# Performance work log

Hardware: AMD Instinct MI355X
Metric: run time of the kernel (lower is better)

The kernel has to match this reference:

```python
import jax, jax.numpy as jnp
import numpy as np

N_NODES = 100000
N_EDGES = 1600000
D_FEAT = 64
UNITS = [128, 128]


def setup_inputs() -> dict:
    key = jax.random.key(0)
    ks = jax.random.split(key, 8)
    row = jax.random.randint(ks[0], (N_EDGES,), 0, N_NODES, dtype=jnp.int32)
    col = jax.random.randint(ks[1], (N_EDGES,), 0, N_NODES, dtype=jnp.int32)
    vals = jax.random.uniform(ks[2], (N_EDGES,), dtype=jnp.float32)
    H = jax.random.normal(ks[3], (N_NODES, D_FEAT), dtype=jnp.float32)
    W1 = jax.random.normal(ks[4], (D_FEAT, UNITS[0]), dtype=jnp.float32) * (1.0 / np.sqrt(D_FEAT))
    b1 = jnp.zeros((UNITS[0],), dtype=jnp.float32)
    W2 = jax.random.normal(ks[5], (UNITS[0], UNITS[1]), dtype=jnp.float32) * (1.0 / np.sqrt(UNITS[0]))
    b2 = jnp.zeros((UNITS[1],), dtype=jnp.float32)
    return {"row": row, "col": col, "vals": vals, "H": H,
            "W1": W1, "b1": b1, "W2": W2, "b2": b2}


def _spmm(row, col, vals, H, n_nodes):
    # sparse A (COO) @ dense H: gather source rows, scale, scatter-add to dest
    return jax.ops.segment_sum(vals[:, None] * H[col], row, num_segments=n_nodes)


def reference(row, col, vals, H, W1, b1, W2, b2):
    n = H.shape[0]
    # layer 0: AH @ W1 + b1, relu (source bug: relu applied since i < num_units-1)
    AH = _spmm(row, col, vals, H, n)
    H1 = jax.nn.relu(AH @ W1 + b1)
    # layer 1: same structure, also relu per source's activation condition
    AH1 = _spmm(row, col, vals, H1, n)
    H2 = jax.nn.relu(AH1 @ W2 + b2)
    return H2
```

## Files before the change

kernel.cpp:

```cpp
#include <hip/hip_runtime.h>


#define NFEAT 64
#define NHID 128
#define BSHIFT 9
#define BROWS (1 << BSHIFT)
#define NB_MAX 256

typedef __attribute__((ext_vector_type(8))) short bf16x8;
typedef __attribute__((ext_vector_type(4))) float f32x4;
typedef __attribute__((ext_vector_type(2))) float f32x2;

__device__ __forceinline__ unsigned short f2bf(float x) {
  unsigned u = __float_as_uint(x);
  unsigned r = (u + 0x7FFFu + ((u >> 16) & 1u)) >> 16;
  return (unsigned short)r;
}
__device__ __forceinline__ unsigned pack2(float a, float b) {
  return (unsigned)f2bf(a) | ((unsigned)f2bf(b) << 16);
}

__device__ __forceinline__ unsigned pk_fp8x4(float a, float b, float c, float d) {
  int w = __builtin_amdgcn_cvt_pk_fp8_f32(a, b, 0, false);
  w = __builtin_amdgcn_cvt_pk_fp8_f32(c, d, w, true);
  return (unsigned)w;
}
__device__ __forceinline__ unsigned char f2fp8(float x) {
  return (unsigned char)(__builtin_amdgcn_cvt_pk_fp8_f32(x, 0.f, 0, false) & 0xFF);
}

__device__ __forceinline__ void acc16(f32x2* a, uint4 q, float v) {
  f32x2 vv = {v, v};
  a[0] += vv * __builtin_amdgcn_cvt_pk_f32_fp8(q.x, false);
  a[1] += vv * __builtin_amdgcn_cvt_pk_f32_fp8(q.x, true);
  a[2] += vv * __builtin_amdgcn_cvt_pk_f32_fp8(q.y, false);
  a[3] += vv * __builtin_amdgcn_cvt_pk_f32_fp8(q.y, true);
  a[4] += vv * __builtin_amdgcn_cvt_pk_f32_fp8(q.z, false);
  a[5] += vv * __builtin_amdgcn_cvt_pk_f32_fp8(q.z, true);
  a[6] += vv * __builtin_amdgcn_cvt_pk_f32_fp8(q.w, false);
  a[7] += vv * __builtin_amdgcn_cvt_pk_f32_fp8(q.w, true);
}

__global__ __launch_bounds__(256) void prep_kernel(
    const float* __restrict__ H, const float* __restrict__ W1,
    const float* __restrict__ W2, unsigned char* __restrict__ Hf8,
    unsigned short* __restrict__ Wsw1, unsigned short* __restrict__ Wsw2,
    int n8) {
  const int total = n8 + 64 * 128 + 128 * 128;
  for (int w = blockIdx.x * 256 + threadIdx.x; w < total; w += gridDim.x * 256) {
    if (w < n8) {
      float4 a = ((const float4*)H)[2 * w];
      float4 b = ((const float4*)H)[2 * w + 1];
      ((uint2*)Hf8)[w] = make_uint2(pk_fp8x4(a.x, a.y, a.z, a.w),
                                    pk_fp8x4(b.x, b.y, b.z, b.w));
    } else {
      int idx = w - n8;
      const float* W = W1;
      unsigned short* Wsw = Wsw1;
      if (idx >= 64 * 128) {
        idx -= 64 * 128;
        W = W2;
        Wsw = Wsw2;
      }
      int j = idx & 7, q = (idx >> 3) & 3, nn = (idx >> 5) & 127, kt = idx >> 12;
      int k = kt * 32 + q * 8 + j;
      Wsw[idx] = f2bf(W[(size_t)k * 128 + nn]);
    }
  }
}

__global__ __launch_bounds__(256) void bhist_kernel(
    const int* __restrict__ row, int* __restrict__ bcnt, int n_edges, int nb) {
  __shared__ int h[NB_MAX];
  for (int i = threadIdx.x; i < NB_MAX; i += 256) h[i] = 0;
  __syncthreads();
  for (int e = blockIdx.x * 256 + threadIdx.x; e < n_edges; e += gridDim.x * 256)
    atomicAdd(&h[row[e] >> BSHIFT], 1);
  __syncthreads();
  for (int i = threadIdx.x; i < nb; i += 256)
    if (h[i]) atomicAdd(&bcnt[i], h[i]);
}

__global__ __launch_bounds__(NB_MAX) void bscan_kernel(
    const int* __restrict__ bcnt, int* __restrict__ bbase, int* __restrict__ cur,
    int* __restrict__ row_ptr, int nb, int n) {
  __shared__ int sm[NB_MAX];
  int t = threadIdx.x;
  int v = (t < nb) ? bcnt[t] : 0;
  sm[t] = v;
  __syncthreads();
  for (int off = 1; off < NB_MAX; off <<= 1) {
    int u = (t >= off) ? sm[t - off] : 0;
    __syncthreads();
    sm[t] += u;
    __syncthreads();
  }
  if (t < nb) {
    bbase[t] = sm[t] - v;
    cur[t] = sm[t] - v;
  }
  if (t == nb - 1) {
    bbase[nb] = sm[t];
    row_ptr[n] = sm[t];
  }
}

__global__ __launch_bounds__(1024) void partition_kernel(
    const int* __restrict__ row, const int* __restrict__ col,
    const float* __restrict__ vals, int* __restrict__ cur,
    int2* __restrict__ bedge, int n_edges) {
  __shared__ int h[NB_MAX], base[NB_MAX], rk[NB_MAX];
  for (int i = threadIdx.x; i < NB_MAX; i += 1024) {
    h[i] = 0;
    rk[i] = 0;
  }
  __syncthreads();
  const int start = blockIdx.x * 1024 + threadIdx.x;
  const int step = gridDim.x * 1024;
  for (int e = start; e < n_edges; e += step)
    atomicAdd(&h[row[e] >> BSHIFT], 1);
  __syncthreads();
  for (int i = threadIdx.x; i < NB_MAX; i += 1024)
    base[i] = h[i] ? atomicAdd(&cur[i], h[i]) : 0;
  __syncthreads();
  for (int e = start; e < n_edges; e += step) {
    int r = row[e];
    int b = r >> BSHIFT;
    int rl = r & (BROWS - 1);
    int p = base[b] + atomicAdd(&rk[b], 1);
    bedge[p] = make_int2((rl << 17) | col[e], __float_as_int(vals[e]));
  }
}

__global__ __launch_bounds__(1024) void bucket_csr_kernel(
    const int* __restrict__ bbase, const int2* __restrict__ bedge,
    int* __restrict__ row_ptr, int2* __restrict__ sedge, int n) {
  __shared__ int cnt[BROWS];
  __shared__ int sm[BROWS];
  const int b = blockIdx.x;
  const int t = threadIdx.x;
  const int beg = bbase[b], end = bbase[b + 1];
  if (t < BROWS) cnt[t] = 0;
  __syncthreads();
  for (int j = beg + t; j < end; j += 1024)
    atomicAdd(&cnt[((unsigned)bedge[j].x) >> 17], 1);
  __syncthreads();
  int v = (t < BROWS) ? cnt[t] : 0;
  if (t < BROWS) sm[t] = v;
  __syncthreads();
  for (int off = 1; off < BROWS; off <<= 1) {
    int u = (t >= off && t < BROWS) ? sm[t - off] : 0;
    __syncthreads();
    if (t < BROWS) sm[t] += u;
    __syncthreads();
  }
  int incl = (t < BROWS) ? sm[t] : 0;
  __syncthreads();
  if (t < BROWS) {
    sm[t] = incl - v;
    int r = (b << BSHIFT) + t;
    if (r < n) row_ptr[r] = beg + sm[t];
    cnt[t] = 0;
  }
  __syncthreads();
  for (int j = beg + t; j < end; j += 1024) {
    int2 ev = bedge[j];
    int rl = ((unsigned)ev.x) >> 17;
    int rank = atomicAdd(&cnt[rl], 1);
    sedge[beg + sm[rl] + rank] = make_int2(ev.x & 0x1FFFF, ev.y);
  }
}

__global__ __launch_bounds__(256) void spmm64_csr_f8(
    const int* __restrict__ row_ptr, const int2* __restrict__ sedge,
    const unsigned char* __restrict__ Hf8, unsigned short* __restrict__ outbf,
    int n) {
  int tid = blockIdx.x * 256 + threadIdx.x;
  int r = tid >> 2;
  int f = tid & 3;
  if (r >= n) return;
  const uint4* Hq = (const uint4*)Hf8;
  int beg = row_ptr[r], end = row_ptr[r + 1];
  f32x2 a[8];
#pragma unroll
  for (int i = 0; i < 8; ++i) a[i] = (f32x2){0.f, 0.f};
  int j = beg;
  if ((j & 1) && j < end) {
    int2 ev = sedge[j];
    uint4 q = Hq[ev.x * 4 + f];
    acc16(a, q, __int_as_float(ev.y));
    ++j;
  }
  for (; j + 4 <= end; j += 4) {
    int4 p0 = ((const int4*)sedge)[j >> 1];
    int4 p1 = ((const int4*)sedge)[(j >> 1) + 1];
    uint4 q0 = Hq[p0.x * 4 + f];
    uint4 q1 = Hq[p0.z * 4 + f];
    uint4 q2 = Hq[p1.x * 4 + f];
    uint4 q3 = Hq[p1.z * 4 + f];
    acc16(a, q0, __int_as_float(p0.y));
    acc16(a, q1, __int_as_float(p0.w));
    acc16(a, q2, __int_as_float(p1.y));
    acc16(a, q3, __int_as_float(p1.w));
  }
  for (; j < end; ++j) {
    int2 ev = sedge[j];
    uint4 q = Hq[ev.x * 4 + f];
    acc16(a, q, __int_as_float(ev.y));
  }
  uint4 o0 = make_uint4(pack2(a[0].x, a[0].y), pack2(a[1].x, a[1].y),
                        pack2(a[2].x, a[2].y), pack2(a[3].x, a[3].y));
  uint4 o1 = make_uint4(pack2(a[4].x, a[4].y), pack2(a[5].x, a[5].y),
                        pack2(a[6].x, a[6].y), pack2(a[7].x, a[7].y));
  ((uint4*)outbf)[(size_t)r * 8 + f * 2] = o0;
  ((uint4*)outbf)[(size_t)r * 8 + f * 2 + 1] = o1;
}

__global__ __launch_bounds__(256) void spmm128_csr_f8(
    const int* __restrict__ row_ptr, const int2* __restrict__ sedge,
    const unsigned char* __restrict__ Hf8, unsigned short* __restrict__ outbf,
    int n) {
  int tid = blockIdx.x * 256 + threadIdx.x;
  int r = tid >> 3;
  int f = tid & 7;
  if (r >= n) return;
  const uint4* Hq = (const uint4*)Hf8;
  int beg = row_ptr[r], end = row_ptr[r + 1];
  f32x2 a[8];
#pragma unroll
  for (int i = 0; i < 8; ++i) a[i] = (f32x2){0.f, 0.f};
  int j = beg;
  if ((j & 1) && j < end) {
    int2 ev = sedge[j];
    uint4 q = Hq[ev.x * 8 + f];
    acc16(a, q, __int_as_float(ev.y));
    ++j;
  }
  for (; j + 4 <= end; j += 4) {
    int4 p0 = ((const int4*)sedge)[j >> 1];
    int4 p1 = ((const int4*)sedge)[(j >> 1) + 1];
    uint4 q0 = Hq[p0.x * 8 + f];
    uint4 q1 = Hq[p0.z * 8 + f];
    uint4 q2 = Hq[p1.x * 8 + f];
    uint4 q3 = Hq[p1.z * 8 + f];
    acc16(a, q0, __int_as_float(p0.y));
    acc16(a, q1, __int_as_float(p0.w));
    acc16(a, q2, __int_as_float(p1.y));
    acc16(a, q3, __int_as_float(p1.w));
  }
  for (; j < end; ++j) {
    int2 ev = sedge[j];
    uint4 q = Hq[ev.x * 8 + f];
    acc16(a, q, __int_as_float(ev.y));
  }
  uint4 o0 = make_uint4(pack2(a[0].x, a[0].y), pack2(a[1].x, a[1].y),
                        pack2(a[2].x, a[2].y), pack2(a[3].x, a[3].y));
  uint4 o1 = make_uint4(pack2(a[4].x, a[4].y), pack2(a[5].x, a[5].y),
                        pack2(a[6].x, a[6].y), pack2(a[7].x, a[7].y));
  ((uint4*)outbf)[(size_t)r * 16 + f * 2] = o0;
  ((uint4*)outbf)[(size_t)r * 16 + f * 2 + 1] = o1;
}

template <int K, int OUTMODE>
__global__ __launch_bounds__(256) void gemm_mfma_relu(
    const unsigned short* __restrict__ Abf,
    const unsigned short* __restrict__ Wsw,
    const float* __restrict__ b, void* __restrict__ out_v, int n) {
  constexpr int KT = K / 32;
  const int lane = threadIdx.x & 63;
  const int wave = threadIdx.x >> 6;
  const int m = lane & 15;
  const int quad = lane >> 4;
  const int r0 = blockIdx.x * 64 + wave * 16;

  bf16x8 bfr[KT][8];
#pragma unroll
  for (int kt = 0; kt < KT; ++kt)
#pragma unroll
    for (int c = 0; c < 8; ++c)
      bfr[kt][c] = *(const bf16x8*)(Wsw + ((size_t)(kt * 128 + c * 16 + m)) * 32 + quad * 8);

  f32x4 acc[8];
#pragma unroll
  for (int c = 0; c < 8; ++c) acc[c] = (f32x4){0.f, 0.f, 0.f, 0.f};

  int row = r0 + m;
  if (row >= n) row = n - 1;
  const uint4* Arow = (const uint4*)(Abf + (size_t)row * K);
#pragma unroll
  for (int kt = 0; kt < KT; ++kt) {
    bf16x8 a = *(const bf16x8*)&Arow[kt * 4 + quad];
#pragma unroll
    for (int c = 0; c < 8; ++c)
      acc[c] = __builtin_amdgcn_mfma_f32_16x16x32_bf16(a, bfr[kt][c], acc[c], 0, 0, 0);
  }

#pragma unroll
  for (int c = 0; c < 8; ++c) {
    float bias = b[c * 16 + m];
#pragma unroll
    for (int i = 0; i < 4; ++i) {
      int rr = r0 + quad * 4 + i;
      if (rr >= n) continue;
      float v = fmaxf(acc[c][i] + bias, 0.f);
      if (OUTMODE == 2)
        ((unsigned char*)out_v)[(size_t)rr * 128 + c * 16 + m] = f2fp8(v);
      else
        ((float*)out_v)[(size_t)rr * 128 + c * 16 + m] = v;
    }
  }
}

__global__ __launch_bounds__(256) void spmm64_atomic(
    const int* __restrict__ row, const int* __restrict__ col,
    const float* __restrict__ vals, const float* __restrict__ Hin,
    float* __restrict__ out, int n_edges) {
  int tid = blockIdx.x * 256 + threadIdx.x;
  int e = tid >> 4, f = tid & 15;
  if (e >= n_edges) return;
  int c = col[e], r = row[e];
  float v = vals[e];
  float4 h = ((const float4*)Hin)[(size_t)c * 16 + f];
  float* o = out + (size_t)r * 64 + f * 4;
  atomicAdd(o + 0, v * h.x);
  atomicAdd(o + 1, v * h.y);
  atomicAdd(o + 2, v * h.z);
  atomicAdd(o + 3, v * h.w);
}

__global__ __launch_bounds__(256) void spmm128_atomic(
    const int* __restrict__ row, const int* __restrict__ col,
    const float* __restrict__ vals, const float* __restrict__ Hin,
    float* __restrict__ out, int n_edges) {
  int tid = blockIdx.x * 256 + threadIdx.x;
  int e = tid >> 5, f = tid & 31;
  if (e >= n_edges) return;
  int c = col[e], r = row[e];
  float v = vals[e];
  float4 h = ((const float4*)Hin)[(size_t)c * 32 + f];
  float* o = out + (size_t)r * 128 + f * 4;
  atomicAdd(o + 0, v * h.x);
  atomicAdd(o + 1, v * h.y);
  atomicAdd(o + 2, v * h.z);
  atomicAdd(o + 3, v * h.w);
}

template <int K>
__global__ __launch_bounds__(256) void gemm_tiled_relu(
    const float* __restrict__ A, const float* __restrict__ W,
    const float* __restrict__ b, float* __restrict__ out, int n) {
  constexpr int KB = 32;
  constexpr int RP = 132;
  __shared__ float As[KB][RP];
  __shared__ float Ws[KB][128];
  const int t = threadIdx.x;
  const int tx = t & 15, ty = t >> 4;
  const int r0 = blockIdx.x * 128;
  float4 acc0[8], acc1[8];
#pragma unroll
  for (int i = 0; i < 8; ++i) {
    acc0[i] = make_float4(0.f, 0.f, 0.f, 0.f);
    acc1[i] = make_float4(0.f, 0.f, 0.f, 0.f);
  }
  for (int k0 = 0; k0 < K; k0 += KB) {
#pragma unroll
    for (int q = 0; q < 4; ++q) {
      int f = q * 256 + t;
      int kk = f >> 5, cv = f & 31;
      ((float4*)&Ws[kk][0])[cv] = ((const float4*)(W + (size_t)(k0 + kk) * 128))[cv];
    }
#pragma unroll
    for (int q = 0; q < 4; ++q) {
      int f = q * 256 + t;
      int r = f >> 3, kv = f & 7;
      float4 av = make_float4(0.f, 0.f, 0.f, 0.f);
      if (r0 + r < n) av = ((const float4*)(A + (size_t)(r0 + r) * K + k0))[kv];
      As[4 * kv + 0][r] = av.x;
      As[4 * kv + 1][r] = av.y;
      As[4 * kv + 2][r] = av.z;
      As[4 * kv + 3][r] = av.w;
    }
    __syncthreads();
#pragma unroll
    for (int k = 0; k < KB; ++k) {
      float4 w0 = *((const float4*)&Ws[k][4 * tx]);
      float4 w1 = *((const float4*)&Ws[k][64 + 4 * tx]);
#pragma unroll
      for (int i = 0; i < 8; ++i) {
        float a = As[k][ty + 16 * i];
        acc0[i].x = fmaf(a, w0.x, acc0[i].x);
        acc0[i].y = fmaf(a, w0.y, acc0[i].y);
        acc0[i].z = fmaf(a, w0.z, acc0[i].z);
        acc0[i].w = fmaf(a, w0.w, acc0[i].w);
        acc1[i].x = fmaf(a, w1.x, acc1[i].x);
        acc1[i].y = fmaf(a, w1.y, acc1[i].y);
        acc1[i].z = fmaf(a, w1.z, acc1[i].z);
        acc1[i].w = fmaf(a, w1.w, acc1[i].w);
      }
    }
    __syncthreads();
  }
  float4 bb0 = ((const float4*)b)[tx];
  float4 bb1 = ((const float4*)(b + 64))[tx];
#pragma unroll
  for (int i = 0; i < 8; ++i) {
    int r = r0 + ty + 16 * i;
    if (r >= n) continue;
    float4 o0, o1;
    o0.x = fmaxf(acc0[i].x + bb0.x, 0.f);
    o0.y = fmaxf(acc0[i].y + bb0.y, 0.f);
    o0.z = fmaxf(acc0[i].z + bb0.z, 0.f);
    o0.w = fmaxf(acc0[i].w + bb0.w, 0.f);
    o1.x = fmaxf(acc1[i].x + bb1.x, 0.f);
    o1.y = fmaxf(acc1[i].y + bb1.y, 0.f);
    o1.z = fmaxf(acc1[i].z + bb1.z, 0.f);
    o1.w = fmaxf(acc1[i].w + bb1.w, 0.f);
    ((float4*)(out + (size_t)r * 128))[tx] = o0;
    ((float4*)(out + (size_t)r * 128 + 64))[tx] = o1;
  }
}

extern "C" void kernel_launch(void* const* d_in, const int* in_sizes, int n_in,
                              void* d_out, int out_size, void* d_ws, size_t ws_size,
                              hipStream_t stream) {
  const int* row = (const int*)d_in[0];
  const int* col = (const int*)d_in[1];
  const float* vals = (const float*)d_in[2];
  const float* H = (const float*)d_in[3];
  const float* W1 = (const float*)d_in[4];
  const float* b1 = (const float*)d_in[5];
  const float* W2 = (const float*)d_in[6];
  const float* b2 = (const float*)d_in[7];
  float* out = (float*)d_out;

  const int n_edges = in_sizes[0];
  const int n_nodes = in_sizes[3] / NFEAT;
  const int nb = (n_nodes + BROWS - 1) / BROWS;
  const int mfma_grid = (n_nodes + 63) / 64;

  size_t off = 0;
  char* base = (char*)d_ws;
  char* slab0 = base;
  size_t slab0_sz = (size_t)n_edges * 8;
  size_t ah1_sz = (size_t)n_nodes * NHID * 2;
  if (ah1_sz > slab0_sz) slab0_sz = ah1_sz;
  off += slab0_sz;
  unsigned char* Hf8 = (unsigned char*)(base + off);   off += (size_t)n_nodes * NFEAT;
  unsigned char* H1f8 = (unsigned char*)(base + off);  off += (size_t)n_nodes * NHID;
  unsigned short* AHbf = (unsigned short*)(base + off); off += (size_t)n_nodes * NFEAT * 2;
  int2* sedge = (int2*)(base + off);  off += (size_t)n_edges * 8;
  unsigned short* Wsw1 = (unsigned short*)(base + off); off += 64 * 128 * 2;
  unsigned short* Wsw2 = (unsigned short*)(base + off); off += 128 * 128 * 2;
  int* bcnt = (int*)(base + off);     off += NB_MAX * 4;
  int* bbase = (int*)(base + off);    off += (NB_MAX + 1) * 4;
  int* cur = (int*)(base + off);      off += NB_MAX * 4;
  int* row_ptr = (int*)(base + off);  off += ((size_t)n_nodes + 1) * 4;
  const size_t needed = off;
  int2* bedge = (int2*)slab0;
  unsigned short* AH1bf = (unsigned short*)slab0;

  if (ws_size >= needed && nb <= NB_MAX && n_nodes <= (1 << 17)) {
    hipMemsetAsync(bcnt, 0, NB_MAX * sizeof(int), stream);
    bhist_kernel<<<1024, 256, 0, stream>>>(row, bcnt, n_edges, nb);
    bscan_kernel<<<1, NB_MAX, 0, stream>>>(bcnt, bbase, cur, row_ptr, nb, n_nodes);
    partition_kernel<<<256, 1024, 0, stream>>>(row, col, vals, cur, bedge, n_edges);
    bucket_csr_kernel<<<nb, 1024, 0, stream>>>(bbase, bedge, row_ptr, sedge, n_nodes);

    prep_kernel<<<1024, 256, 0, stream>>>(H, W1, W2, Hf8, Wsw1, Wsw2,
                                          n_nodes * NFEAT / 8);

    spmm64_csr_f8<<<(n_nodes * 4 + 255) / 256, 256, 0, stream>>>(
        row_ptr, sedge, Hf8, AHbf, n_nodes);
    gemm_mfma_relu<64, 2><<<mfma_grid, 256, 0, stream>>>(
        AHbf, Wsw1, b1, H1f8, n_nodes);
    spmm128_csr_f8<<<(n_nodes * 8 + 255) / 256, 256, 0, stream>>>(
        row_ptr, sedge, H1f8, AH1bf, n_nodes);
    gemm_mfma_relu<128, 0><<<mfma_grid, 256, 0, stream>>>(
        AH1bf, Wsw2, b2, out, n_nodes);
  } else {
    float* fAH = (float*)d_ws;
    float* fH1 = fAH + (size_t)n_nodes * NFEAT;
    hipMemsetAsync(fAH, 0, (size_t)n_nodes * NFEAT * sizeof(float), stream);
    hipMemsetAsync(out, 0, (size_t)n_nodes * NHID * sizeof(float), stream);
    spmm64_atomic<<<(n_edges * 16 + 255) / 256, 256, 0, stream>>>(row, col, vals, H, fAH, n_edges);
    gemm_tiled_relu<64><<<(n_nodes + 127) / 128, 256, 0, stream>>>(fAH, W1, b1, fH1, n_nodes);
    spmm128_atomic<<<(n_edges * 32 + 255) / 256, 256, 0, stream>>>(row, col, vals, fH1, out, n_edges);
    gemm_tiled_relu<128><<<(n_nodes + 127) / 128, 256, 0, stream>>>(out, W2, b2, out, n_nodes);
  }
}
```

Measured before the change: 281.5 us.

## Fuse SpMM gather with MFMA GEMM via shared-memory tile per layer

```diff
diff --git a/kernel.cpp b/kernel.cpp
--- a/kernel.cpp
+++ b/kernel.cpp
@@ -39,6 +39,34 @@
   a[5] += vv * __builtin_amdgcn_cvt_pk_f32_fp8(q.z, true);
   a[6] += vv * __builtin_amdgcn_cvt_pk_f32_fp8(q.w, false);
   a[7] += vv * __builtin_amdgcn_cvt_pk_f32_fp8(q.w, true);
+}
+
+template <int RS>
+__device__ __forceinline__ void gather_row(
+    const int2* __restrict__ sedge, const uint4* __restrict__ Hq,
+    int beg, int end, int f, f32x2* a) {
+  int j = beg;
+  if ((j & 1) && j < end) {
+    int2 ev = sedge[j];
+    acc16(a, Hq[ev.x * RS + f], __int_as_float(ev.y));
+    ++j;
+  }
+  for (; j + 4 <= end; j += 4) {
+    int4 p0 = ((const int4*)sedge)[j >> 1];
+    int4 p1 = ((const int4*)sedge)[(j >> 1) + 1];
+    uint4 q0 = Hq[p0.x * RS + f];
+    uint4 q1 = Hq[p0.z * RS + f];
+    uint4 q2 = Hq[p1.x * RS + f];
+    uint4 q3 = Hq[p1.z * RS + f];
+    acc16(a, q0, __int_as_float(p0.y));
+    acc16(a, q1, __int_as_float(p0.w));
+    acc16(a, q2, __int_as_float(p1.y));
+    acc16(a, q3, __int_as_float(p1.w));
+  }
+  for (; j < end; ++j) {
+    int2 ev = sedge[j];
+    acc16(a, Hq[ev.x * RS + f], __int_as_float(ev.y));
+  }
 }
 
 __global__ __launch_bounds__(256) void prep_kernel(
@@ -74,8 +102,16 @@
   __shared__ int h[NB_MAX];
   for (int i = threadIdx.x; i < NB_MAX; i += 256) h[i] = 0;
   __syncthreads();
-  for (int e = blockIdx.x * 256 + threadIdx.x; e < n_edges; e += gridDim.x * 256)
-    atomicAdd(&h[row[e] >> BSHIFT], 1);
+  const int n4 = n_edges >> 2;
+  for (int i = blockIdx.x * 256 + threadIdx.x; i < n4; i += gridDim.x * 256) {
+    int4 r4 = ((const int4*)row)[i];
+    atomicAdd(&h[r4.x >> BSHIFT], 1);
+    atomicAdd(&h[r4.y >> BSHIFT], 1);
+    atomicAdd(&h[r4.z >> BSHIFT], 1);
+    atomicAdd(&h[r4.w >> BSHIFT], 1);
+  }
+  if (blockIdx.x == 0 && threadIdx.x < (n_edges & 3))
+    atomicAdd(&h[row[(n4 << 2) + threadIdx.x] >> BSHIFT], 1);
   __syncthreads();
   for (int i = threadIdx.x; i < nb; i += 256)
     if (h[i]) atomicAdd(&bcnt[i], h[i]);
@@ -171,130 +207,52 @@
   }
 }
 
-__global__ __launch_bounds__(256) void spmm64_csr_f8(
+__global__ __launch_bounds__(256) void fused64_kernel(
     const int* __restrict__ row_ptr, const int2* __restrict__ sedge,
-    const unsigned char* __restrict__ Hf8, unsigned short* __restrict__ outbf,
-    int n) {
-  int tid = blockIdx.x * 256 + threadIdx.x;
-  int r = tid >> 2;
-  int f = tid & 3;
-  if (r >= n) return;
-  const uint4* Hq = (const uint4*)Hf8;
-  int beg = row_ptr[r], end = row_ptr[r + 1];
-  f32x2 a[8];
-#pragma unroll
-  for (int i = 0; i < 8; ++i) a[i] = (f32x2){0.f, 0.f};
-  int j = beg;
-  if ((j & 1) && j < end) {
-    int2 ev = sedge[j];
-    uint4 q = Hq[ev.x * 4 + f];
-    acc16(a, q, __int_as_float(ev.y));
-    ++j;
-  }
-  for (; j + 4 <= end; j += 4) {
-    int4 p0 = ((const int4*)sedge)[j >> 1];
-    int4 p1 = ((const int4*)sedge)[(j >> 1) + 1];
-    uint4 q0 = Hq[p0.x * 4 + f];
-    uint4 q1 = Hq[p0.z * 4 + f];
-    uint4 q2 = Hq[p1.x * 4 + f];
-    uint4 q3 = Hq[p1.z * 4 + f];
-    acc16(a, q0, __int_as_float(p0.y));
-    acc16(a, q1, __int_as_float(p0.w));
-    acc16(a, q2, __int_as_float(p1.y));
-    acc16(a, q3, __int_as_float(p1.w));
-  }
-  for (; j < end; ++j) {
-    int2 ev = sedge[j];
-    uint4 q = Hq[ev.x * 4 + f];
-    acc16(a, q, __int_as_float(ev.y));
-  }
-  uint4 o0 = make_uint4(pack2(a[0].x, a[0].y), pack2(a[1].x, a[1].y),
-                        pack2(a[2].x, a[2].y), pack2(a[3].x, a[3].y));
-  uint4 o1 = make_uint4(pack2(a[4].x, a[4].y), pack2(a[5].x, a[5].y),
-                        pack2(a[6].x, a[6].y), pack2(a[7].x, a[7].y));
-  ((uint4*)outbf)[(size_t)r * 8 + f * 2] = o0;
-  ((uint4*)outbf)[(size_t)r * 8 + f * 2 + 1] = o1;
-}
-
-__global__ __launch_bounds__(256) void spmm128_csr_f8(
-    const int* __restrict__ row_ptr, const int2* __restrict__ sedge,
-    const unsigned char* __restrict__ Hf8, unsigned short* __restrict__ outbf,
-    int n) {
-  int tid = blockIdx.x * 256 + threadIdx.x;
-  int r = tid >> 3;
-  int f = tid & 7;
-  if (r >= n) return;
-  const uint4* Hq = (const uint4*)Hf8;
-  int beg = row_ptr[r], end = row_ptr[r + 1];
-  f32x2 a[8];
-#pragma unroll
-  for (int i = 0; i < 8; ++i) a[i] = (f32x2){0.f, 0.f};
-  int j = beg;
-  if ((j & 1) && j < end) {
-    int2 ev = sedge[j];
-    uint4 q = Hq[ev.x * 8 + f];
-    acc16(a, q, __int_as_float(ev.y));
-    ++j;
-  }
-  for (; j + 4 <= end; j += 4) {
-    int4 p0 = ((const int4*)sedge)[j >> 1];
-    int4 p1 = ((const int4*)sedge)[(j >> 1) + 1];
-    uint4 q0 = Hq[p0.x * 8 + f];
-    uint4 q1 = Hq[p0.z * 8 + f];
-    uint4 q2 = Hq[p1.x * 8 + f];
-    uint4 q3 = Hq[p1.z * 8 + f];
-    acc16(a, q0, __int_as_float(p0.y));
-    acc16(a, q1, __int_as_float(p0.w));
-    acc16(a, q2, __int_as_float(p1.y));
-    acc16(a, q3, __int_as_float(p1.w));
-  }
-  for (; j < end; ++j) {
-    int2 ev = sedge[j];
-    uint4 q = Hq[ev.x * 8 + f];
-    acc16(a, q, __int_as_float(ev.y));
-  }
-  uint4 o0 = make_uint4(pack2(a[0].x, a[0].y), pack2(a[1].x, a[1].y),
-                        pack2(a[2].x, a[2].y), pack2(a[3].x, a[3].y));
-  uint4 o1 = make_uint4(pack2(a[4].x, a[4].y), pack2(a[5].x, a[5].y),
-                        pack2(a[6].x, a[6].y), pack2(a[7].x, a[7].y));
-  ((uint4*)outbf)[(size_t)r * 16 + f * 2] = o0;
-  ((uint4*)outbf)[(size_t)r * 16 + f * 2 + 1] = o1;
-}
-
-template <int K, int OUTMODE>
-__global__ __launch_bounds__(256) void gemm_mfma_relu(
-    const unsigned short* __restrict__ Abf,
+    const unsigned char* __restrict__ Hf8,
     const unsigned short* __restrict__ Wsw,
-    const float* __restrict__ b, void* __restrict__ out_v, int n) {
-  constexpr int KT = K / 32;
-  const int lane = threadIdx.x & 63;
-  const int wave = threadIdx.x >> 6;
-  const int m = lane & 15;
-  const int quad = lane >> 4;
-  const int r0 = blockIdx.x * 64 + wave * 16;
-
-  bf16x8 bfr[KT][8];
-#pragma unroll
-  for (int kt = 0; kt < KT; ++kt)
+    const float* __restrict__ b, unsigned char* __restrict__ H1f8, int n) {
+  __shared__ uint4 tile[64 * 9];
+  const int tid = threadIdx.x;
+  {
+    const int rl = tid >> 2, f = tid & 3;
+    const int r = blockIdx.x * 64 + rl;
+    int beg = 0, end = 0;
+    if (r < n) {
+      beg = row_ptr[r];
+      end = row_ptr[r + 1];
+    }
+    f32x2 a[8];
+#pragma unroll
+    for (int i = 0; i < 8; ++i) a[i] = (f32x2){0.f, 0.f};
+    gather_row<4>(sedge, (const uint4*)Hf8, beg, end, f, a);
+    tile[rl * 9 + f * 2] =
+        make_uint4(pack2(a[0].x, a[0].y), pack2(a[1].x, a[1].y),
+                   pack2(a[2].x, a[2].y), pack2(a[3].x, a[3].y));
+    tile[rl * 9 + f * 2 + 1] =
+        make_uint4(pack2(a[4].x, a[4].y), pack2(a[5].x, a[5].y),
+                   pack2(a[6].x, a[6].y), pack2(a[7].x, a[7].y));
+  }
+  const int lane = tid & 63, wave = tid >> 6;
+  const int m = lane & 15, quad = lane >> 4;
+  bf16x8 bfr[2][8];
+#pragma unroll
+  for (int kt = 0; kt < 2; ++kt)
 #pragma unroll
     for (int c = 0; c < 8; ++c)
       bfr[kt][c] = *(const bf16x8*)(Wsw + ((size_t)(kt * 128 + c * 16 + m)) * 32 + quad * 8);
-
+  __syncthreads();
   f32x4 acc[8];
 #pragma unroll
   for (int c = 0; c < 8; ++c) acc[c] = (f32x4){0.f, 0.f, 0.f, 0.f};
-
-  int row = r0 + m;
-  if (row >= n) row = n - 1;
-  const uint4* Arow = (const uint4*)(Abf + (size_t)row * K);
-#pragma unroll
-  for (int kt = 0; kt < KT; ++kt) {
-    bf16x8 a = *(const bf16x8*)&Arow[kt * 4 + quad];
+#pragma unroll
+  for (int kt = 0; kt < 2; ++kt) {
+    bf16x8 a = *(const bf16x8*)&tile[(wave * 16 + m) * 9 + kt * 4 + quad];
 #pragma unroll
     for (int c = 0; c < 8; ++c)
       acc[c] = __builtin_amdgcn_mfma_f32_16x16x32_bf16(a, bfr[kt][c], acc[c], 0, 0, 0);
   }
-
+  const int r0 = blockIdx.x * 64 + wave * 16;
 #pragma unroll
   for (int c = 0; c < 8; ++c) {
     float bias = b[c * 16 + m];
@@ -302,11 +260,66 @@
     for (int i = 0; i < 4; ++i) {
       int rr = r0 + quad * 4 + i;
       if (rr >= n) continue;
-      float v = fmaxf(acc[c][i] + bias, 0.f);
-      if (OUTMODE == 2)
-        ((unsigned char*)out_v)[(size_t)rr * 128 + c * 16 + m] = f2fp8(v);
-      else
-        ((float*)out_v)[(size_t)rr * 128 + c * 16 + m] = v;
+      H1f8[(size_t)rr * 128 + c * 16 + m] = f2fp8(fmaxf(acc[c][i] + bias, 0.f));
+    }
+  }
+}
+
+__global__ __launch_bounds__(512) void fused128_kernel(
+    const int* __restrict__ row_ptr, const int2* __restrict__ sedge,
+    const unsigned char* __restrict__ H1f8,
+    const unsigned short* __restrict__ Wsw,
+    const float* __restrict__ b, float* __restrict__ out, int n) {
+  __shared__ uint4 tile[64 * 17];
+  const int tid = threadIdx.x;
+  {
+    const int rl = tid >> 3, f = tid & 7;
+    const int r = blockIdx.x * 64 + rl;
+    int beg = 0, end = 0;
+    if (r < n) {
+      beg = row_ptr[r];
+      end = row_ptr[r + 1];
+    }
+    f32x2 a[8];
+#pragma unroll
+    for (int i = 0; i < 8; ++i) a[i] = (f32x2){0.f, 0.f};
+    gather_row<8>(sedge, (const uint4*)H1f8, beg, end, f, a);
+    tile[rl * 17 + f * 2] =
+        make_uint4(pack2(a[0].x, a[0].y), pack2(a[1].x, a[1].y),
+                   pack2(a[2].x, a[2].y), pack2(a[3].x, a[3].y));
+    tile[rl * 17 + f * 2 + 1] =
+        make_uint4(pack2(a[4].x, a[4].y), pack2(a[5].x, a[5].y),
+                   pack2(a[6].x, a[6].y), pack2(a[7].x, a[7].y));
+  }
+  const int lane = tid & 63, wave = tid >> 6;
+  const int m = lane & 15, quad = lane >> 4;
+  const int g = wave >> 1, h = wave & 1;
+  bf16x8 bfr[4][4];
+#pragma unroll
+  for (int kt = 0; kt < 4; ++kt)
+#pragma unroll
+    for (int c = 0; c < 4; ++c)
+      bfr[kt][c] = *(const bf16x8*)(Wsw + ((size_t)(kt * 128 + (h * 4 + c) * 16 + m)) * 32 + quad * 8);
+  __syncthreads();
+  f32x4 acc[4];
+#pragma unroll
+  for (int c = 0; c < 4; ++c) acc[c] = (f32x4){0.f, 0.f, 0.f, 0.f};
+#pragma unroll
+  for (int kt = 0; kt < 4; ++kt) {
+    bf16x8 a = *(const bf16x8*)&tile[(g * 16 + m) * 17 + kt * 4 + quad];
+#pragma unroll
+    for (int c = 0; c < 4; ++c)
+      acc[c] = __builtin_amdgcn_mfma_f32_16x16x32_bf16(a, bfr[kt][c], acc[c], 0, 0, 0);
+  }
+  const int r0 = blockIdx.x * 64 + g * 16;
+#pragma unroll
+  for (int c = 0; c < 4; ++c) {
+    float bias = b[(h * 4 + c) * 16 + m];
+#pragma unroll
+    for (int i = 0; i < 4; ++i) {
+      int rr = r0 + quad * 4 + i;
+      if (rr >= n) continue;
+      out[(size_t)rr * 128 + (h * 4 + c) * 16 + m] = fmaxf(acc[c][i] + bias, 0.f);
     }
   }
 }
@@ -436,18 +449,13 @@
   const int n_edges = in_sizes[0];
   const int n_nodes = in_sizes[3] / NFEAT;
   const int nb = (n_nodes + BROWS - 1) / BROWS;
-  const int mfma_grid = (n_nodes + 63) / 64;
+  const int fused_grid = (n_nodes + 63) / 64;
 
   size_t off = 0;
   char* base = (char*)d_ws;
-  char* slab0 = base;
-  size_t slab0_sz = (size_t)n_edges * 8;
-  size_t ah1_sz = (size_t)n_nodes * NHID * 2;
-  if (ah1_sz > slab0_sz) slab0_sz = ah1_sz;
-  off += slab0_sz;
+  int2* bedge = (int2*)(base + off);  off += (size_t)n_edges * 8;
   unsigned char* Hf8 = (unsigned char*)(base + off);   off += (size_t)n_nodes * NFEAT;
   unsigned char* H1f8 = (unsigned char*)(base + off);  off += (size_t)n_nodes * NHID;
-  unsigned short* AHbf = (unsigned short*)(base + off); off += (size_t)n_nodes * NFEAT * 2;
   int2* sedge = (int2*)(base + off);  off += (size_t)n_edges * 8;
   unsigned short* Wsw1 = (unsigned short*)(base + off); off += 64 * 128 * 2;
   unsigned short* Wsw2 = (unsigned short*)(base + off); off += 128 * 128 * 2;
@@ -456,8 +464,6 @@
   int* cur = (int*)(base + off);      off += NB_MAX * 4;
   int* row_ptr = (int*)(base + off);  off += ((size_t)n_nodes + 1) * 4;
   const size_t needed = off;
-  int2* bedge = (int2*)slab0;
-  unsigned short* AH1bf = (unsigned short*)slab0;
 
   if (ws_size >= needed && nb <= NB_MAX && n_nodes <= (1 << 17)) {
     hipMemsetAsync(bcnt, 0, NB_MAX * sizeof(int), stream);
@@ -469,14 +475,10 @@
     prep_kernel<<<1024, 256, 0, stream>>>(H, W1, W2, Hf8, Wsw1, Wsw2,
                                           n_nodes * NFEAT / 8);
 
-    spmm64_csr_f8<<<(n_nodes * 4 + 255) / 256, 256, 0, stream>>>(
-        row_ptr, sedge, Hf8, AHbf, n_nodes);
-    gemm_mfma_relu<64, 2><<<mfma_grid, 256, 0, stream>>>(
-        AHbf, Wsw1, b1, H1f8, n_nodes);
-    spmm128_csr_f8<<<(n_nodes * 8 + 255) / 256, 256, 0, stream>>>(
-        row_ptr, sedge, H1f8, AH1bf, n_nodes);
-    gemm_mfma_relu<128, 0><<<mfma_grid, 256, 0, stream>>>(
-        AH1bf, Wsw2, b2, out, n_nodes);
+    fused64_kernel<<<fused_grid, 256, 0, stream>>>(
+        row_ptr, sedge, Hf8, Wsw1, b1, H1f8, n_nodes);
+    fused128_kernel<<<fused_grid, 512, 0, stream>>>(
+        row_ptr, sedge, H1f8, Wsw2, b2, out, n_nodes);
   } else {
     float* fAH = (float*)d_ws;
     float* fH1 = fAH + (size_t)n_nodes * NFEAT;
```

Result: faster. 271.7 us (-3.5%).
